# Performance work log

Measured on AMD Instinct MI355X. Metric: run time of the kernel, lower is better.

Reference implementation:

```python
import jax, jax.numpy as jnp
import numpy as np

FILTS = 100  # conv padding = aconv_filts
SCALING = 2.0


def setup_inputs() -> dict:
    key = jax.random.key(0)
    ks = jax.random.split(key, 9)
    T, DUNITS, ATT, EPROJ, CH, K = 50000, 1024, 512, 512, 10, 2 * FILTS + 1
    return {
        "dec_z": jax.random.normal(ks[0], (1, DUNITS), jnp.float32),
        "att_prev": jax.random.uniform(ks[1], (1, T), jnp.float32),
        "pre_compute_enc_h": jax.random.normal(ks[2], (1, T, ATT), jnp.float32),
        "enc_h": jax.random.normal(ks[3], (1, T, EPROJ), jnp.float32),
        "mask": jnp.zeros((1, T), jnp.float32),
        "conv_w": jax.random.normal(ks[4], (CH, 1, K), jnp.float32) * 0.05,
        "w_att": jax.random.normal(ks[5], (ATT, CH), jnp.float32) * 0.05,
        "w_dec": jax.random.normal(ks[6], (ATT, DUNITS), jnp.float32) * 0.02,
        "w_gvec": jax.random.normal(ks[7], (1, ATT), jnp.float32) * 0.05,
        "b_gvec": jnp.zeros((1,), jnp.float32),
    }


def reference(dec_z, att_prev, pre_compute_enc_h, enc_h, mask, conv_w, w_att, w_dec, w_gvec, b_gvec):
    # loc_conv: 1-channel 1D conv over previous attention weights -> [1, CH, T]
    att_conv = jax.lax.conv_general_dilated(
        att_prev[:, None, :], conv_w, window_strides=(1,),
        padding=[(FILTS, FILTS)], dimension_numbers=("NCH", "OIH", "NCH"))
    # mlp_att: [1, T, ATT]
    att_conv = jnp.einsum("bct,ac->bta", att_conv, w_att)
    # mlp_dec, tiled over frames: [1, 1, ATT]
    dec_tiled = (dec_z @ w_dec.T)[:, None, :]
    # gvec(tanh(...)) -> scores e: [1, T]
    e = jnp.einsum("bta,a->bt", jnp.tanh(att_conv + pre_compute_enc_h + dec_tiled), w_gvec[0]) + b_gvec
    e = e + mask
    w = jax.nn.softmax(SCALING * e, axis=1)  # [1, T]
    c = jnp.sum(enc_h * w[..., None], axis=1)  # [1, EPROJ]
    return (c, w)
```

## Files before the change

### kernel.cpp

```cpp
#include <hip/hip_runtime.h>
#include <math.h>


constexpr int ATT    = 512;
constexpr int CH     = 10;
constexpr int PCH    = 12;
constexpr int KW     = 201;
constexpr int FILTS  = 100;
constexpr int DUNITS = 1024;
constexpr int NB1    = 1024;
constexpr int NB3    = 1024;
constexpr int CT     = 64;
constexpr float SCALING = 2.0f;

__device__ __forceinline__ float wave_reduce_sum(float v) {
    #pragma unroll
    for (int off = 32; off > 0; off >>= 1) v += __shfl_xor(v, off, 64);
    return v;
}

__device__ __forceinline__ float fast_tanh(float x) {
    x = fminf(fmaxf(x, -15.f), 15.f);
    float e = __expf(2.f * x);
    return __fdividef(e - 1.f, e + 1.f);
}

__global__ __launch_bounds__(256, 4) void k0_conv_dec(
    const float* __restrict__ att_prev,
    const float* __restrict__ conv_w,
    const float* __restrict__ dec_z,
    const float* __restrict__ w_dec,
    float* __restrict__ ws_aconv,
    float* __restrict__ ws_dec,
    float* __restrict__ out,
    int T, int nbconv)
{
    if ((int)blockIdx.x < nbconv) {
        __shared__ float s_ap[CT + KW - 1];
        __shared__ float s_wt[KW * 12];
        __shared__ float s_part[4 * CT * CH];
        const int t0 = blockIdx.x * CT;
        for (int i = threadIdx.x; i < CT + KW - 1; i += 256) {
            int t = t0 - FILTS + i;
            s_ap[i] = (t >= 0 && t < T) ? att_prev[t] : 0.f;
        }
        for (int i = threadIdx.x; i < CH * KW; i += 256) {
            int c = i % CH, k = i / CH;
            s_wt[k * 12 + c] = conv_w[c * KW + k];
        }
        __syncthreads();
        const int tl = threadIdx.x & 63;
        const int kq = threadIdx.x >> 6;
        float acc[CH];
        #pragma unroll
        for (int c = 0; c < CH; ++c) acc[c] = 0.f;
        for (int k = kq; k < KW; k += 4) {
            float x = s_ap[tl + k];
            const float4 w0 = *(const float4*)&s_wt[k * 12];
            const float4 w1 = *(const float4*)&s_wt[k * 12 + 4];
            const float2 w2 = *(const float2*)&s_wt[k * 12 + 8];
            acc[0] += x * w0.x; acc[1] += x * w0.y;
            acc[2] += x * w0.z; acc[3] += x * w0.w;
            acc[4] += x * w1.x; acc[5] += x * w1.y;
            acc[6] += x * w1.z; acc[7] += x * w1.w;
            acc[8] += x * w2.x; acc[9] += x * w2.y;
        }
        #pragma unroll
        for (int c = 0; c < CH; ++c) s_part[kq * (CT * CH) + tl * CH + c] = acc[c];
        __syncthreads();
        for (int idx = threadIdx.x; idx < CT * PCH; idx += 256) {
            int t = idx / PCH, c = idx % PCH;
            float v = 0.f;
            if (c < CH) {
                int j = t * CH + c;
                v = s_part[j] + s_part[CT * CH + j]
                  + s_part[2 * CT * CH + j] + s_part[3 * CT * CH + j];
            }
            if (t0 + t < T) ws_aconv[(size_t)(t0 + t) * PCH + c] = v;
        }
    } else {
        const int b    = blockIdx.x - nbconv;
        const int wid  = threadIdx.x >> 6;
        const int lane = threadIdx.x & 63;
        const int a    = b * 4 + wid;
        if (threadIdx.x < 4) out[b * 4 + threadIdx.x] = 0.f;
        const float4* wd = (const float4*)(w_dec + (size_t)a * DUNITS);
        const float4* dz = (const float4*)dec_z;
        float acc = 0.f;
        #pragma unroll
        for (int q = 0; q < 4; ++q) {
            float4 wv = wd[lane + q * 64];
            float4 zv = dz[lane + q * 64];
            acc += wv.x * zv.x + wv.y * zv.y + wv.z * zv.z + wv.w * zv.w;
        }
        acc = wave_reduce_sum(acc);
        if (lane == 0) ws_dec[a] = acc;
    }
}

__global__ __launch_bounds__(256, 3) void k1_scores(
    const float* __restrict__ pre,
    const float* __restrict__ mask,
    const float* __restrict__ w_att,
    const float* __restrict__ w_gvec,
    const float* __restrict__ b_gvec,
    const float* __restrict__ ws_dec,
    const float* __restrict__ ws_aconv,
    float* __restrict__ ws_e,
    float* __restrict__ ws_ms,
    int T)
{
    __shared__ float s_watt[ATT * CH];
    __shared__ float s_m[4], s_s[4];
    for (int i = threadIdx.x; i < ATT * CH; i += 256) s_watt[i] = w_att[i];
    __syncthreads();

    const int wid  = threadIdx.x >> 6;
    const int lane = threadIdx.x & 63;

    float wa[8][CH];
    #pragma unroll
    for (int j = 0; j < 4; ++j) {
        #pragma unroll
        for (int c = 0; c < CH; ++c) {
            wa[j][c]     = s_watt[(lane * 4 + j) * CH + c];
            wa[4 + j][c] = s_watt[(256 + lane * 4 + j) * CH + c];
        }
    }
    const float4 dlo = ((const float4*)ws_dec)[lane];
    const float4 dhi = ((const float4*)ws_dec)[64 + lane];
    const float4 glo = ((const float4*)w_gvec)[lane];
    const float4 ghi = ((const float4*)w_gvec)[64 + lane];
    const float  bg  = b_gvec[0];

    float m = -INFINITY, s = 0.f;
    const float4* pre4 = (const float4*)pre;
    const float4* ac4  = (const float4*)ws_aconv;
    const int gw = blockIdx.x * 4 + wid;

    for (int tb = gw * 4; tb < T; tb += NB1 * 4 * 4) {
        float4 p0[4], p1[4];
        float  msk[4];
        #pragma unroll
        for (int i = 0; i < 4; ++i) {
            int t = tb + i;
            if (t < T) {
                p0[i]  = pre4[(size_t)t * 128 + lane];
                p1[i]  = pre4[(size_t)t * 128 + 64 + lane];
                msk[i] = mask[t];
            }
        }
        #pragma unroll
        for (int i = 0; i < 4; ++i) {
            int t = tb + i;
            if (t >= T) break;
            float ac[12];
            *(float4*)&ac[0] = ac4[(size_t)t * 3 + 0];
            *(float4*)&ac[4] = ac4[(size_t)t * 3 + 1];
            *(float4*)&ac[8] = ac4[(size_t)t * 3 + 2];
            float av[8];
            #pragma unroll
            for (int j = 0; j < 8; ++j) {
                float v = 0.f;
                #pragma unroll
                for (int c = 0; c < CH; ++c) v += ac[c] * wa[j][c];
                av[j] = v;
            }
            float x0 = fast_tanh(p0[i].x + dlo.x + av[0]);
            float x1 = fast_tanh(p0[i].y + dlo.y + av[1]);
            float x2 = fast_tanh(p0[i].z + dlo.z + av[2]);
            float x3 = fast_tanh(p0[i].w + dlo.w + av[3]);
            float x4 = fast_tanh(p1[i].x + dhi.x + av[4]);
            float x5 = fast_tanh(p1[i].y + dhi.y + av[5]);
            float x6 = fast_tanh(p1[i].z + dhi.z + av[6]);
            float x7 = fast_tanh(p1[i].w + dhi.w + av[7]);
            float acc = glo.x * x0 + glo.y * x1 + glo.z * x2 + glo.w * x3
                      + ghi.x * x4 + ghi.y * x5 + ghi.z * x6 + ghi.w * x7;
            acc = wave_reduce_sum(acc);
            float y = SCALING * (acc + bg + msk[i]);
            if (lane == 0) ws_e[t] = y;
            float nm = fmaxf(m, y);
            s = s * __expf(m - nm) + __expf(y - nm);
            m = nm;
        }
    }
    if (lane == 0) { s_m[wid] = m; s_s[wid] = s; }
    __syncthreads();
    if (threadIdx.x == 0) {
        float M = s_m[0], S = s_s[0];
        #pragma unroll
        for (int w = 1; w < 4; ++w) {
            float m2 = s_m[w], s2 = s_s[w];
            float nm = fmaxf(M, m2);
            S = S * __expf(M - nm) + s2 * __expf(m2 - nm);
            M = nm;
        }
        ws_ms[blockIdx.x * 2]     = M;
        ws_ms[blockIdx.x * 2 + 1] = S;
    }
}

__global__ __launch_bounds__(256, 4) void k3_ctx(
    const float* __restrict__ enc_h,
    const float* __restrict__ ws_e,
    const float* __restrict__ ws_ms,
    float* __restrict__ out,
    int T)
{
    __shared__ float s_m[256], s_s[256];
    {
        float m = -INFINITY, s = 0.f;
        for (int i = threadIdx.x; i < NB1; i += 256) {
            float m2 = ws_ms[i * 2], s2 = ws_ms[i * 2 + 1];
            float nm = fmaxf(m, m2);
            s = s * __expf(m - nm) + s2 * __expf(m2 - nm);
            m = nm;
        }
        s_m[threadIdx.x] = m; s_s[threadIdx.x] = s;
        __syncthreads();
        for (int off = 128; off > 0; off >>= 1) {
            if ((int)threadIdx.x < off) {
                float M = s_m[threadIdx.x], S = s_s[threadIdx.x];
                float m2 = s_m[threadIdx.x + off], s2 = s_s[threadIdx.x + off];
                float nm = fmaxf(M, m2);
                s_s[threadIdx.x] = S * __expf(M - nm) + s2 * __expf(m2 - nm);
                s_m[threadIdx.x] = nm;
            }
            __syncthreads();
        }
    }
    const float M  = s_m[0];
    const float IS = 1.f / s_s[0];

    const int wid  = threadIdx.x >> 6;
    const int lane = threadIdx.x & 63;
    const float4* eh4 = (const float4*)enc_h;

    float4 a0 = make_float4(0.f, 0.f, 0.f, 0.f);
    float4 a1 = make_float4(0.f, 0.f, 0.f, 0.f);
    const int gw = blockIdx.x * 4 + wid;

    for (int tb = gw * 4; tb < T; tb += NB3 * 4 * 4) {
        float4 e0[4], e1[4];
        float  y[4];
        #pragma unroll
        for (int i = 0; i < 4; ++i) {
            int t = tb + i;
            if (t < T) {
                e0[i] = eh4[(size_t)t * 128 + lane];
                e1[i] = eh4[(size_t)t * 128 + 64 + lane];
                y[i]  = ws_e[t];
            }
        }
        #pragma unroll
        for (int i = 0; i < 4; ++i) {
            int t = tb + i;
            if (t >= T) break;
            float w = __expf(y[i] - M) * IS;
            if (lane == 0) out[ATT + t] = w;
            a0.x += w * e0[i].x; a0.y += w * e0[i].y;
            a0.z += w * e0[i].z; a0.w += w * e0[i].w;
            a1.x += w * e1[i].x; a1.y += w * e1[i].y;
            a1.z += w * e1[i].z; a1.w += w * e1[i].w;
        }
    }

    __shared__ float4 s_c[4 * 128];
    s_c[wid * 128 + lane]      = a0;
    s_c[wid * 128 + 64 + lane] = a1;
    __syncthreads();
    const float* sc = (const float*)s_c;
    for (int a = threadIdx.x; a < ATT; a += 256) {
        float v = sc[a] + sc[512 + a] + sc[1024 + a] + sc[1536 + a];
        atomicAdd(&out[a], v);
    }
}

extern "C" void kernel_launch(void* const* d_in, const int* in_sizes, int n_in,
                              void* d_out, int out_size, void* d_ws, size_t ws_size,
                              hipStream_t stream)
{
    const float* dec_z    = (const float*)d_in[0];
    const float* att_prev = (const float*)d_in[1];
    const float* pre      = (const float*)d_in[2];
    const float* enc_h    = (const float*)d_in[3];
    const float* mask     = (const float*)d_in[4];
    const float* conv_w   = (const float*)d_in[5];
    const float* w_att    = (const float*)d_in[6];
    const float* w_dec    = (const float*)d_in[7];
    const float* w_gvec   = (const float*)d_in[8];
    const float* b_gvec   = (const float*)d_in[9];
    const int T = in_sizes[1];

    float* ws       = (float*)d_ws;
    float* ws_dec   = ws;
    float* ws_aconv = ws_dec + ATT;
    float* ws_e     = ws_aconv + (size_t)T * PCH;
    float* ws_ms    = ws_e + T;
    float* out      = (float*)d_out;

    const int nbconv = (T + CT - 1) / CT;

    hipLaunchKernelGGL(k0_conv_dec, dim3(nbconv + ATT / 4), dim3(256), 0, stream,
                       att_prev, conv_w, dec_z, w_dec, ws_aconv, ws_dec, out, T, nbconv);
    hipLaunchKernelGGL(k1_scores, dim3(NB1), dim3(256), 0, stream,
                       pre, mask, w_att, w_gvec, b_gvec, ws_dec, ws_aconv,
                       ws_e, ws_ms, T);
    hipLaunchKernelGGL(k3_ctx, dim3(NB3), dim3(256), 0, stream,
                       enc_h, ws_e, ws_ms, out, T);
}
```

Measured before the change: 273.5 us.

## Fuse three attention kernels into one persistent kernel with grid barriers

Merges the conv/dec, score/softmax-stat, and context kernels into a single persistent launch of 512 blocks. The phases are separated by atomic-counter grid barriers, and a memset resets the counter before launch. This removes two kernel launch gaps and loads the conv weights once per block instead of once per tile. In exchange it gives up the overlap between stages, depends on all 512 blocks being co-resident, and adds spin-wait barrier latency and a memset call.

Result: slower. 390.9 us (+42.9%).

```diff
diff --git a/kernel.cpp b/kernel.cpp
--- a/kernel.cpp
+++ b/kernel.cpp
@@ -8,8 +8,7 @@
 constexpr int KW     = 201;
 constexpr int FILTS  = 100;
 constexpr int DUNITS = 1024;
-constexpr int NB1    = 1024;
-constexpr int NB3    = 1024;
+constexpr int NBLK   = 512;
 constexpr int CT     = 64;
 constexpr float SCALING = 2.0f;
 
@@ -25,40 +24,77 @@
     return __fdividef(e - 1.f, e + 1.f);
 }
 
-__global__ __launch_bounds__(256, 4) void k0_conv_dec(
+struct ConvS {
+    float ap[CT + KW - 1];
+    float wt[KW * 12];
+    float part[4 * CT * CH];
+};
+
+union alignas(16) ShU {
+    ConvS conv;
+    float watt[ATT * CH];
+    float c[4 * ATT];
+};
+
+__device__ __forceinline__ void grid_barrier(unsigned* bar, unsigned target) {
+    __syncthreads();
+    if (threadIdx.x == 0) {
+        __threadfence();
+        atomicAdd(bar, 1u);
+        while (__hip_atomic_load(bar, __ATOMIC_ACQUIRE,
+                                 __HIP_MEMORY_SCOPE_AGENT) < target)
+            __builtin_amdgcn_s_sleep(2);
+        __threadfence();
+    }
+    __syncthreads();
+}
+
+__global__ __launch_bounds__(256, 2) void fused_attloc(
+    const float* __restrict__ dec_z,
     const float* __restrict__ att_prev,
+    const float* __restrict__ pre,
+    const float* __restrict__ enc_h,
+    const float* __restrict__ mask,
     const float* __restrict__ conv_w,
-    const float* __restrict__ dec_z,
+    const float* __restrict__ w_att,
     const float* __restrict__ w_dec,
+    const float* __restrict__ w_gvec,
+    const float* __restrict__ b_gvec,
+    float* __restrict__ out,
+    float* __restrict__ ws_dec,
     float* __restrict__ ws_aconv,
-    float* __restrict__ ws_dec,
-    float* __restrict__ out,
+    float* __restrict__ ws_e,
+    float* __restrict__ ws_ms,
+    unsigned* __restrict__ bar,
     int T, int nbconv)
 {
-    if ((int)blockIdx.x < nbconv) {
-        __shared__ float s_ap[CT + KW - 1];
-        __shared__ float s_wt[KW * 12];
-        __shared__ float s_part[4 * CT * CH];
-        const int t0 = blockIdx.x * CT;
-        for (int i = threadIdx.x; i < CT + KW - 1; i += 256) {
+    __shared__ ShU u;
+    __shared__ float s_m[256], s_s[256];
+    const int tid  = threadIdx.x;
+    const int bid  = blockIdx.x;
+    const int wid  = tid >> 6;
+    const int lane = tid & 63;
+
+    for (int i = tid; i < CH * KW; i += 256) {
+        int c = i % CH, k = i / CH;
+        u.conv.wt[k * 12 + c] = conv_w[c * KW + k];
+    }
+    for (int tile = bid; tile < nbconv; tile += NBLK) {
+        const int t0 = tile * CT;
+        __syncthreads();
+        for (int i = tid; i < CT + KW - 1; i += 256) {
             int t = t0 - FILTS + i;
-            s_ap[i] = (t >= 0 && t < T) ? att_prev[t] : 0.f;
-        }
-        for (int i = threadIdx.x; i < CH * KW; i += 256) {
-            int c = i % CH, k = i / CH;
-            s_wt[k * 12 + c] = conv_w[c * KW + k];
+            u.conv.ap[i] = (t >= 0 && t < T) ? att_prev[t] : 0.f;
         }
         __syncthreads();
-        const int tl = threadIdx.x & 63;
-        const int kq = threadIdx.x >> 6;
         float acc[CH];
         #pragma unroll
         for (int c = 0; c < CH; ++c) acc[c] = 0.f;
-        for (int k = kq; k < KW; k += 4) {
-            float x = s_ap[tl + k];
-            const float4 w0 = *(const float4*)&s_wt[k * 12];
-            const float4 w1 = *(const float4*)&s_wt[k * 12 + 4];
-            const float2 w2 = *(const float2*)&s_wt[k * 12 + 8];
+        for (int k = wid; k < KW; k += 4) {
+            float x = u.conv.ap[lane + k];
+            const float4 w0 = *(const float4*)&u.conv.wt[k * 12];
+            const float4 w1 = *(const float4*)&u.conv.wt[k * 12 + 4];
+            const float2 w2 = *(const float2*)&u.conv.wt[k * 12 + 8];
             acc[0] += x * w0.x; acc[1] += x * w0.y;
             acc[2] += x * w0.z; acc[3] += x * w0.w;
             acc[4] += x * w1.x; acc[5] += x * w1.y;
@@ -66,24 +102,22 @@
             acc[8] += x * w2.x; acc[9] += x * w2.y;
         }
         #pragma unroll
-        for (int c = 0; c < CH; ++c) s_part[kq * (CT * CH) + tl * CH + c] = acc[c];
+        for (int c = 0; c < CH; ++c)
+            u.conv.part[wid * (CT * CH) + lane * CH + c] = acc[c];
         __syncthreads();
-        for (int idx = threadIdx.x; idx < CT * PCH; idx += 256) {
-            int t = idx / PCH, c = idx % PCH;
+        for (int idx = tid; idx < CT * PCH; idx += 256) {
+            int tt = idx / PCH, c = idx % PCH;
             float v = 0.f;
             if (c < CH) {
-                int j = t * CH + c;
-                v = s_part[j] + s_part[CT * CH + j]
-                  + s_part[2 * CT * CH + j] + s_part[3 * CT * CH + j];
-            }
-            if (t0 + t < T) ws_aconv[(size_t)(t0 + t) * PCH + c] = v;
-        }
-    } else {
-        const int b    = blockIdx.x - nbconv;
-        const int wid  = threadIdx.x >> 6;
-        const int lane = threadIdx.x & 63;
-        const int a    = b * 4 + wid;
-        if (threadIdx.x < 4) out[b * 4 + threadIdx.x] = 0.f;
+                int j = tt * CH + c;
+                v = u.conv.part[j] + u.conv.part[CT * CH + j]
+                  + u.conv.part[2 * CT * CH + j] + u.conv.part[3 * CT * CH + j];
+            }
+            if (t0 + tt < T) ws_aconv[(size_t)(t0 + tt) * PCH + c] = v;
+        }
+    }
+    if (bid < ATT / 4) {
+        const int a = bid * 4 + wid;
         const float4* wd = (const float4*)(w_dec + (size_t)a * DUNITS);
         const float4* dz = (const float4*)dec_z;
         float acc = 0.f;
@@ -96,35 +130,21 @@
         acc = wave_reduce_sum(acc);
         if (lane == 0) ws_dec[a] = acc;
     }
-}
-
-__global__ __launch_bounds__(256, 3) void k1_scores(
-    const float* __restrict__ pre,
-    const float* __restrict__ mask,
-    const float* __restrict__ w_att,
-    const float* __restrict__ w_gvec,
-    const float* __restrict__ b_gvec,
-    const float* __restrict__ ws_dec,
-    const float* __restrict__ ws_aconv,
-    float* __restrict__ ws_e,
-    float* __restrict__ ws_ms,
-    int T)
-{
-    __shared__ float s_watt[ATT * CH];
-    __shared__ float s_m[4], s_s[4];
-    for (int i = threadIdx.x; i < ATT * CH; i += 256) s_watt[i] = w_att[i];
-    __syncthreads();
-
-    const int wid  = threadIdx.x >> 6;
-    const int lane = threadIdx.x & 63;
+    if (bid == NBLK - 1)
+        for (int i = tid; i < ATT; i += 256) out[i] = 0.f;
+
+    grid_barrier(bar, NBLK);
+
+    for (int i = tid; i < ATT * CH; i += 256) u.watt[i] = w_att[i];
+    __syncthreads();
 
     float wa[8][CH];
     #pragma unroll
     for (int j = 0; j < 4; ++j) {
         #pragma unroll
         for (int c = 0; c < CH; ++c) {
-            wa[j][c]     = s_watt[(lane * 4 + j) * CH + c];
-            wa[4 + j][c] = s_watt[(256 + lane * 4 + j) * CH + c];
+            wa[j][c]     = u.watt[(lane * 4 + j) * CH + c];
+            wa[4 + j][c] = u.watt[(256 + lane * 4 + j) * CH + c];
         }
     }
     const float4 dlo = ((const float4*)ws_dec)[lane];
@@ -136,9 +156,9 @@
     float m = -INFINITY, s = 0.f;
     const float4* pre4 = (const float4*)pre;
     const float4* ac4  = (const float4*)ws_aconv;
-    const int gw = blockIdx.x * 4 + wid;
-
-    for (int tb = gw * 4; tb < T; tb += NB1 * 4 * 4) {
+    const int gw = bid * 4 + wid;
+
+    for (int tb = gw * 4; tb < T; tb += NBLK * 16) {
         float4 p0[4], p1[4];
         float  msk[4];
         #pragma unroll
@@ -186,7 +206,7 @@
     }
     if (lane == 0) { s_m[wid] = m; s_s[wid] = s; }
     __syncthreads();
-    if (threadIdx.x == 0) {
+    if (tid == 0) {
         float M = s_m[0], S = s_s[0];
         #pragma unroll
         for (int w = 1; w < 4; ++w) {
@@ -195,36 +215,29 @@
             S = S * __expf(M - nm) + s2 * __expf(m2 - nm);
             M = nm;
         }
-        ws_ms[blockIdx.x * 2]     = M;
-        ws_ms[blockIdx.x * 2 + 1] = S;
-    }
-}
-
-__global__ __launch_bounds__(256, 4) void k3_ctx(
-    const float* __restrict__ enc_h,
-    const float* __restrict__ ws_e,
-    const float* __restrict__ ws_ms,
-    float* __restrict__ out,
-    int T)
-{
-    __shared__ float s_m[256], s_s[256];
+        ws_ms[bid * 2]     = M;
+        ws_ms[bid * 2 + 1] = S;
+    }
+
+    grid_barrier(bar, 2 * NBLK);
+
     {
-        float m = -INFINITY, s = 0.f;
-        for (int i = threadIdx.x; i < NB1; i += 256) {
+        float mm = -INFINITY, ss = 0.f;
+        for (int i = tid; i < NBLK; i += 256) {
             float m2 = ws_ms[i * 2], s2 = ws_ms[i * 2 + 1];
-            float nm = fmaxf(m, m2);
-            s = s * __expf(m - nm) + s2 * __expf(m2 - nm);
-            m = nm;
-        }
-        s_m[threadIdx.x] = m; s_s[threadIdx.x] = s;
+            float nm = fmaxf(mm, m2);
+            ss = ss * __expf(mm - nm) + s2 * __expf(m2 - nm);
+            mm = nm;
+        }
+        s_m[tid] = mm; s_s[tid] = ss;
         __syncthreads();
         for (int off = 128; off > 0; off >>= 1) {
-            if ((int)threadIdx.x < off) {
-                float M = s_m[threadIdx.x], S = s_s[threadIdx.x];
-                float m2 = s_m[threadIdx.x + off], s2 = s_s[threadIdx.x + off];
-                float nm = fmaxf(M, m2);
-                s_s[threadIdx.x] = S * __expf(M - nm) + s2 * __expf(m2 - nm);
-                s_m[threadIdx.x] = nm;
+            if (tid < off) {
+                float M1 = s_m[tid], S1 = s_s[tid];
+                float m2 = s_m[tid + off], s2 = s_s[tid + off];
+                float nm = fmaxf(M1, m2);
+                s_s[tid] = S1 * __expf(M1 - nm) + s2 * __expf(m2 - nm);
+                s_m[tid] = nm;
             }
             __syncthreads();
         }
@@ -232,15 +245,11 @@
     const float M  = s_m[0];
     const float IS = 1.f / s_s[0];
 
-    const int wid  = threadIdx.x >> 6;
-    const int lane = threadIdx.x & 63;
-    const float4* eh4 = (const float4*)enc_h;
-
     float4 a0 = make_float4(0.f, 0.f, 0.f, 0.f);
     float4 a1 = make_float4(0.f, 0.f, 0.f, 0.f);
-    const int gw = blockIdx.x * 4 + wid;
-
-    for (int tb = gw * 4; tb < T; tb += NB3 * 4 * 4) {
+    const float4* eh4 = (const float4*)enc_h;
+
+    for (int tb = gw * 4; tb < T; tb += NBLK * 16) {
         float4 e0[4], e1[4];
         float  y[4];
         #pragma unroll
@@ -265,12 +274,13 @@
         }
     }
 
-    __shared__ float4 s_c[4 * 128];
-    s_c[wid * 128 + lane]      = a0;
-    s_c[wid * 128 + 64 + lane] = a1;
-    __syncthreads();
-    const float* sc = (const float*)s_c;
-    for (int a = threadIdx.x; a < ATT; a += 256) {
+    __syncthreads();
+    float4* s_c4 = (float4*)u.c;
+    s_c4[wid * 128 + lane]      = a0;
+    s_c4[wid * 128 + 64 + lane] = a1;
+    __syncthreads();
+    const float* sc = u.c;
+    for (int a = tid; a < ATT; a += 256) {
         float v = sc[a] + sc[512 + a] + sc[1024 + a] + sc[1536 + a];
         atomicAdd(&out[a], v);
     }
@@ -292,7 +302,8 @@
     const float* b_gvec   = (const float*)d_in[9];
     const int T = in_sizes[1];
 
-    float* ws       = (float*)d_ws;
+    unsigned* bar   = (unsigned*)d_ws;
+    float* ws       = (float*)d_ws + 16;
     float* ws_dec   = ws;
     float* ws_aconv = ws_dec + ATT;
     float* ws_e     = ws_aconv + (size_t)T * PCH;
@@ -301,11 +312,9 @@
 
     const int nbconv = (T + CT - 1) / CT;
 
-    hipLaunchKernelGGL(k0_conv_dec, dim3(nbconv + ATT / 4), dim3(256), 0, stream,
-                       att_prev, conv_w, dec_z, w_dec, ws_aconv, ws_dec, out, T, nbconv);
-    hipLaunchKernelGGL(k1_scores, dim3(NB1), dim3(256), 0, stream,
-                       pre, mask, w_att, w_gvec, b_gvec, ws_dec, ws_aconv,
-                       ws_e, ws_ms, T);
-    hipLaunchKernelGGL(k3_ctx, dim3(NB3), dim3(256), 0, stream,
-                       enc_h, ws_e, ws_ms, out, T);
-}
+    hipMemsetAsync(bar, 0, 64, stream);
+    hipLaunchKernelGGL(fused_attloc, dim3(NBLK), dim3(256), 0, stream,
+                       dec_z, att_prev, pre, enc_h, mask, conv_w, w_att, w_dec,
+                       w_gvec, b_gvec, out, ws_dec, ws_aconv, ws_e, ws_ms,
+                       bar, T, nbconv);
+}
```

## Software-pipeline score and context loops with double-buffered register prefetch

Applied to the files above, without the earlier changes.

Both the scores and context kernels now run a fixed four-batch loop. The next batch of pre_compute_enc_h/enc_h rows is loaded into a second register buffer while the current batch is computed, so global-load latency overlaps with tanh and FMA work. The scores kernel also batches the online-softmax update over four frames, reads w_att straight from global memory instead of staging it in shared memory, and relaxes launch bounds to two blocks per SM so more registers are available. The tanh clamp is dropped for a form that saturates safely without it. The cost is higher register pressure and lower occupancy, and the hardcoded four batches only cover T up to 4*16384.

Result: slower. 299.0 us (+9.3%).

```diff
diff --git a/kernel.cpp b/kernel.cpp
--- a/kernel.cpp
+++ b/kernel.cpp
@@ -20,9 +20,8 @@
 }
 
 __device__ __forceinline__ float fast_tanh(float x) {
-    x = fminf(fmaxf(x, -15.f), 15.f);
     float e = __expf(2.f * x);
-    return __fdividef(e - 1.f, e + 1.f);
+    return 1.f - __fdividef(2.f, e + 1.f);
 }
 
 __global__ __launch_bounds__(256, 4) void k0_conv_dec(
@@ -98,7 +97,7 @@
     }
 }
 
-__global__ __launch_bounds__(256, 3) void k1_scores(
+__global__ __launch_bounds__(256, 2) void k1_scores(
     const float* __restrict__ pre,
     const float* __restrict__ mask,
     const float* __restrict__ w_att,
@@ -110,11 +109,7 @@
     float* __restrict__ ws_ms,
     int T)
 {
-    __shared__ float s_watt[ATT * CH];
     __shared__ float s_m[4], s_s[4];
-    for (int i = threadIdx.x; i < ATT * CH; i += 256) s_watt[i] = w_att[i];
-    __syncthreads();
-
     const int wid  = threadIdx.x >> 6;
     const int lane = threadIdx.x & 63;
 
@@ -123,8 +118,8 @@
     for (int j = 0; j < 4; ++j) {
         #pragma unroll
         for (int c = 0; c < CH; ++c) {
-            wa[j][c]     = s_watt[(lane * 4 + j) * CH + c];
-            wa[4 + j][c] = s_watt[(256 + lane * 4 + j) * CH + c];
+            wa[j][c]     = w_att[(lane * 4 + j) * CH + c];
+            wa[4 + j][c] = w_att[(256 + lane * 4 + j) * CH + c];
         }
     }
     const float4 dlo = ((const float4*)ws_dec)[lane];
@@ -133,70 +128,100 @@
     const float4 ghi = ((const float4*)w_gvec)[64 + lane];
     const float  bg  = b_gvec[0];
 
-    float m = -INFINITY, s = 0.f;
     const float4* pre4 = (const float4*)pre;
     const float4* ac4  = (const float4*)ws_aconv;
     const int gw = blockIdx.x * 4 + wid;
-
-    for (int tb = gw * 4; tb < T; tb += NB1 * 4 * 4) {
-        float4 p0[4], p1[4];
-        float  msk[4];
+    const int t0 = gw * 4;
+    constexpr int S = NB1 * 16;
+
+    float m = -INFINITY, s = 0.f;
+    float4 pA0[4], pA1[4], pB0[4], pB1[4];
+    float  mA[4], mB[4];
+    float4 acx[4], acy[4], acz[4];
+
+    auto loadp = [&](float4 (&P0)[4], float4 (&P1)[4], float (&MSK)[4], int tb) {
         #pragma unroll
         for (int i = 0; i < 4; ++i) {
             int t = tb + i;
             if (t < T) {
-                p0[i]  = pre4[(size_t)t * 128 + lane];
-                p1[i]  = pre4[(size_t)t * 128 + 64 + lane];
-                msk[i] = mask[t];
-            }
-        }
+                P0[i]  = pre4[(size_t)t * 128 + lane];
+                P1[i]  = pre4[(size_t)t * 128 + 64 + lane];
+                MSK[i] = mask[t];
+            }
+        }
+    };
+    auto loada = [&](int tb) {
         #pragma unroll
         for (int i = 0; i < 4; ++i) {
             int t = tb + i;
-            if (t >= T) break;
-            float ac[12];
-            *(float4*)&ac[0] = ac4[(size_t)t * 3 + 0];
-            *(float4*)&ac[4] = ac4[(size_t)t * 3 + 1];
-            *(float4*)&ac[8] = ac4[(size_t)t * 3 + 2];
-            float av[8];
-            #pragma unroll
-            for (int j = 0; j < 8; ++j) {
-                float v = 0.f;
-                #pragma unroll
-                for (int c = 0; c < CH; ++c) v += ac[c] * wa[j][c];
-                av[j] = v;
-            }
-            float x0 = fast_tanh(p0[i].x + dlo.x + av[0]);
-            float x1 = fast_tanh(p0[i].y + dlo.y + av[1]);
-            float x2 = fast_tanh(p0[i].z + dlo.z + av[2]);
-            float x3 = fast_tanh(p0[i].w + dlo.w + av[3]);
-            float x4 = fast_tanh(p1[i].x + dhi.x + av[4]);
-            float x5 = fast_tanh(p1[i].y + dhi.y + av[5]);
-            float x6 = fast_tanh(p1[i].z + dhi.z + av[6]);
-            float x7 = fast_tanh(p1[i].w + dhi.w + av[7]);
-            float acc = glo.x * x0 + glo.y * x1 + glo.z * x2 + glo.w * x3
-                      + ghi.x * x4 + ghi.y * x5 + ghi.z * x6 + ghi.w * x7;
-            acc = wave_reduce_sum(acc);
-            float y = SCALING * (acc + bg + msk[i]);
-            if (lane == 0) ws_e[t] = y;
-            float nm = fmaxf(m, y);
-            s = s * __expf(m - nm) + __expf(y - nm);
-            m = nm;
-        }
-    }
+            if (t < T) {
+                acx[i] = ac4[(size_t)t * 3 + 0];
+                acy[i] = ac4[(size_t)t * 3 + 1];
+                acz[i] = ac4[(size_t)t * 3 + 2];
+            }
+        }
+    };
+    auto batch = [&](float4 (&P0)[4], float4 (&P1)[4], float (&MSK)[4], int tb,
+                     float4 (&NP0)[4], float4 (&NP1)[4], float (&NM)[4], int tn,
+                     bool pf) {
+        if (pf) loadp(NP0, NP1, NM, tn);
+        float y[4];
+        #pragma unroll
+        for (int i = 0; i < 4; ++i) {
+            const int t = tb + i;
+            y[i] = -INFINITY;
+            if (t < T) {
+                const float4 a0 = acx[i], a1 = acy[i], a2 = acz[i];
+                float x0 = P0[i].x + dlo.x, x1 = P0[i].y + dlo.y;
+                float x2 = P0[i].z + dlo.z, x3 = P0[i].w + dlo.w;
+                float x4 = P1[i].x + dhi.x, x5 = P1[i].y + dhi.y;
+                float x6 = P1[i].z + dhi.z, x7 = P1[i].w + dhi.w;
+                #define AV(X, J) \
+                    X += a0.x*wa[J][0] + a0.y*wa[J][1] + a0.z*wa[J][2] + a0.w*wa[J][3] \
+                       + a1.x*wa[J][4] + a1.y*wa[J][5] + a1.z*wa[J][6] + a1.w*wa[J][7] \
+                       + a2.x*wa[J][8] + a2.y*wa[J][9]
+                AV(x0, 0); AV(x1, 1); AV(x2, 2); AV(x3, 3);
+                AV(x4, 4); AV(x5, 5); AV(x6, 6); AV(x7, 7);
+                #undef AV
+                float acc = glo.x * fast_tanh(x0) + glo.y * fast_tanh(x1)
+                          + glo.z * fast_tanh(x2) + glo.w * fast_tanh(x3)
+                          + ghi.x * fast_tanh(x4) + ghi.y * fast_tanh(x5)
+                          + ghi.z * fast_tanh(x6) + ghi.w * fast_tanh(x7);
+                acc = wave_reduce_sum(acc);
+                float yy = SCALING * (acc + bg + MSK[i]);
+                if (lane == 0) ws_e[t] = yy;
+                y[i] = yy;
+            }
+        }
+        if (pf) loada(tn);
+        float ymax = fmaxf(fmaxf(y[0], y[1]), fmaxf(y[2], y[3]));
+        float nm = fmaxf(m, ymax);
+        float add = __expf(y[0] - nm) + __expf(y[1] - nm)
+                  + __expf(y[2] - nm) + __expf(y[3] - nm);
+        s = s * __expf(m - nm) + add;
+        m = nm;
+    };
+
+    loadp(pA0, pA1, mA, t0);
+    loada(t0);
+    batch(pA0, pA1, mA, t0,         pB0, pB1, mB, t0 + S,     true);
+    batch(pB0, pB1, mB, t0 + S,     pA0, pA1, mA, t0 + 2 * S, true);
+    batch(pA0, pA1, mA, t0 + 2 * S, pB0, pB1, mB, t0 + 3 * S, true);
+    batch(pB0, pB1, mB, t0 + 3 * S, pA0, pA1, mA, 0,          false);
+
     if (lane == 0) { s_m[wid] = m; s_s[wid] = s; }
     __syncthreads();
     if (threadIdx.x == 0) {
-        float M = s_m[0], S = s_s[0];
+        float M = s_m[0], Ssum = s_s[0];
         #pragma unroll
         for (int w = 1; w < 4; ++w) {
             float m2 = s_m[w], s2 = s_s[w];
             float nm = fmaxf(M, m2);
-            S = S * __expf(M - nm) + s2 * __expf(m2 - nm);
+            Ssum = Ssum * __expf(M - nm) + s2 * __expf(m2 - nm);
             M = nm;
         }
         ws_ms[blockIdx.x * 2]     = M;
-        ws_ms[blockIdx.x * 2 + 1] = S;
+        ws_ms[blockIdx.x * 2 + 1] = Ssum;
     }
 }
 
@@ -220,10 +245,10 @@
         __syncthreads();
         for (int off = 128; off > 0; off >>= 1) {
             if ((int)threadIdx.x < off) {
-                float M = s_m[threadIdx.x], S = s_s[threadIdx.x];
+                float M1 = s_m[threadIdx.x], S1 = s_s[threadIdx.x];
                 float m2 = s_m[threadIdx.x + off], s2 = s_s[threadIdx.x + off];
-                float nm = fmaxf(M, m2);
-                s_s[threadIdx.x] = S * __expf(M - nm) + s2 * __expf(m2 - nm);
+                float nm = fmaxf(M1, m2);
+                s_s[threadIdx.x] = S1 * __expf(M1 - nm) + s2 * __expf(m2 - nm);
                 s_m[threadIdx.x] = nm;
             }
             __syncthreads();
@@ -235,36 +260,51 @@
     const int wid  = threadIdx.x >> 6;
     const int lane = threadIdx.x & 63;
     const float4* eh4 = (const float4*)enc_h;
+    const int gw = blockIdx.x * 4 + wid;
+    const int t0 = gw * 4;
+    constexpr int S = NB3 * 16;
 
     float4 a0 = make_float4(0.f, 0.f, 0.f, 0.f);
     float4 a1 = make_float4(0.f, 0.f, 0.f, 0.f);
-    const int gw = blockIdx.x * 4 + wid;
-
-    for (int tb = gw * 4; tb < T; tb += NB3 * 4 * 4) {
-        float4 e0[4], e1[4];
-        float  y[4];
+    float4 eA0[4], eA1[4], eB0[4], eB1[4];
+    float  yA[4], yB[4];
+
+    auto loade = [&](float4 (&E0)[4], float4 (&E1)[4], float (&Y)[4], int tb) {
         #pragma unroll
         for (int i = 0; i < 4; ++i) {
             int t = tb + i;
             if (t < T) {
-                e0[i] = eh4[(size_t)t * 128 + lane];
-                e1[i] = eh4[(size_t)t * 128 + 64 + lane];
-                y[i]  = ws_e[t];
-            }
-        }
+                E0[i] = eh4[(size_t)t * 128 + lane];
+                E1[i] = eh4[(size_t)t * 128 + 64 + lane];
+                Y[i]  = ws_e[t];
+            }
+        }
+    };
+    auto batch = [&](float4 (&E0)[4], float4 (&E1)[4], float (&Y)[4], int tb,
+                     float4 (&NE0)[4], float4 (&NE1)[4], float (&NY)[4], int tn,
+                     bool pf) {
+        if (pf) loade(NE0, NE1, NY, tn);
         #pragma unroll
         for (int i = 0; i < 4; ++i) {
             int t = tb + i;
-            if (t >= T) break;
-            float w = __expf(y[i] - M) * IS;
-            if (lane == 0) out[ATT + t] = w;
-            a0.x += w * e0[i].x; a0.y += w * e0[i].y;
-            a0.z += w * e0[i].z; a0.w += w * e0[i].w;
-            a1.x += w * e1[i].x; a1.y += w * e1[i].y;
-            a1.z += w * e1[i].z; a1.w += w * e1[i].w;
-        }
-    }
-
+            if (t < T) {
+                float w = __expf(Y[i] - M) * IS;
+                if (lane == 0) out[ATT + t] = w;
+                a0.x += w * E0[i].x; a0.y += w * E0[i].y;
+                a0.z += w * E0[i].z; a0.w += w * E0[i].w;
+                a1.x += w * E1[i].x; a1.y += w * E1[i].y;
+                a1.z += w * E1[i].z; a1.w += w * E1[i].w;
+            }
+        }
+    };
+
+    loade(eA0, eA1, yA, t0);
+    batch(eA0, eA1, yA, t0,         eB0, eB1, yB, t0 + S,     true);
+    batch(eB0, eB1, yB, t0 + S,     eA0, eA1, yA, t0 + 2 * S, true);
+    batch(eA0, eA1, yA, t0 + 2 * S, eB0, eB1, yB, t0 + 3 * S, true);
+    batch(eB0, eB1, yB, t0 + 3 * S, eA0, eA1, yA, 0,          false);
+
+    __syncthreads();
     __shared__ float4 s_c[4 * 128];
     s_c[wid * 128 + lane]      = a0;
     s_c[wid * 128 + 64 + lane] = a1;
```
